# Optimization experiments

Hardware: AMD Instinct MI355X
Metric: run time of the kernel (lower is better)

Reference implementation:

```python
import jax, jax.numpy as jnp
import numpy as np

B, C, H, W, K = 16, 64, 256, 256, 3

def setup_inputs() -> dict:
    key = jax.random.key(0)
    ks = jax.random.split(key, 3)
    x = jax.random.normal(ks[0], (B, C, H, W), dtype=jnp.float32)
    # ReDistribution params
    rd_k = jnp.ones((1, C, 1, 1), jnp.float32)
    rd_b = jnp.zeros((1, C, 1, 1), jnp.float32)
    # Spectral binary activation beta
    beta = jnp.ones((1,), jnp.float32)
    # HardBinaryConv real-valued latent weights (Conv2d default init scale)
    fan_in = C * K * K
    bound = 1.0 / np.sqrt(fan_in)
    conv_w = jax.random.uniform(ks[1], (C, C, K, K), jnp.float32, -bound, bound)
    # RPReLU params
    pr_bias0 = jnp.zeros((1, C, 1, 1), jnp.float32)
    prelu_w = jnp.full((C,), 0.25, jnp.float32)
    pr_bias1 = jnp.zeros((1, C, 1, 1), jnp.float32)
    return {"x": x, "rd_k": rd_k, "rd_b": rd_b, "beta": beta,
            "conv_w": conv_w, "pr_bias0": pr_bias0, "prelu_w": prelu_w,
            "pr_bias1": pr_bias1}

def _ste(hard, soft):
    # straight-through estimator: forward=hard, backward grads flow via soft
    return jax.lax.stop_gradient(hard - soft) + soft

def reference(x, rd_k, rd_b, beta, conv_w, pr_bias0, prelu_w, pr_bias1):
    sg = jax.lax.stop_gradient
    # ReDistribution
    out = x * rd_k + rd_b
    # Spectral binary activation with tanh STE
    out = _ste(jnp.sign(out), jnp.tanh(out * beta))
    # HardBinaryConv: per-output-channel mean |w| scaling, sign binarize, clip STE
    scaling = sg(jnp.mean(jnp.abs(conv_w), axis=(1, 2, 3), keepdims=True))  # [C,1,1,1]
    bw = _ste(scaling * jnp.sign(conv_w), jnp.clip(conv_w, -1.0, 1.0))
    y = jax.lax.conv_general_dilated(
        out, bw, window_strides=(1, 1), padding=((1, 1), (1, 1)),
        dimension_numbers=("NCHW", "OIHW", "NCHW"))
    # RPReLU: bias0 -> per-channel PReLU -> bias1
    y = y + pr_bias0
    y = jnp.where(y >= 0, y, prelu_w[None, :, None, None] * y)
    y = y + pr_bias1
    return y + x
```

## Files before the change

### kernel.cpp

```cpp
#include <hip/hip_runtime.h>
#include <cstdint>
#include <cstddef>

#define Bn 16
#define Cn 64
#define Hn 256
#define Wn 256
#define HWn (Hn * Wn)
#define TH 8
#define ROWS (TH + 2)
#define COLS (Wn + 2)
#define NBLK (Bn * (Hn / TH))
#define THREADS 1024

typedef unsigned long long u64;
typedef u64   u64x2 __attribute__((ext_vector_type(2)));
typedef float f32x2 __attribute__((ext_vector_type(2)));
typedef float f32x4 __attribute__((ext_vector_type(4)));

__global__ __launch_bounds__(64) void pack_weights(const float* __restrict__ w,
                                                   const float* __restrict__ b0g,
                                                   const float* __restrict__ pwg,
                                                   const float* __restrict__ b1g,
                                                   u64* __restrict__ wbits,
                                                   float4* __restrict__ par,
                                                   int* __restrict__ corrx) {
    const int co = blockIdx.x;
    const int ci = threadIdx.x;
    const float* wp = w + ((size_t)co * Cn + ci) * 9;
    float v[9];
    float asum = 0.f;
    #pragma unroll
    for (int t = 0; t < 9; ++t) { v[t] = wp[t]; asum += fabsf(v[t]); }
    u64 m[9];
    #pragma unroll
    for (int t = 0; t < 9; ++t) m[t] = __ballot(v[t] > 0.f);
    #pragma unroll
    for (int off = 32; off; off >>= 1) asum += __shfl_xor(asum, off);
    if (ci == 0) {
        int c[9];
        #pragma unroll
        for (int t = 0; t < 9; ++t) {
            wbits[co * 9 + t] = m[t];
            c[t] = 64 - 2 * (int)__popcll(m[t]);
        }
        int* cx = corrx + co * 8;
        cx[0] = c[0] + c[1] + c[2];
        cx[1] = c[6] + c[7] + c[8];
        cx[2] = c[0] + c[3] + c[6];
        cx[3] = c[2] + c[5] + c[8];
        cx[4] = c[0]; cx[5] = c[2];
        cx[6] = c[6]; cx[7] = c[8];
        par[co] = make_float4(asum * (1.f / (Cn * 9)), b0g[co], pwg[co], b1g[co]);
    }
}

__global__ __launch_bounds__(THREADS, 2) void fused(const float* __restrict__ x,
                                                    const float* __restrict__ rdk,
                                                    const float* __restrict__ rdb,
                                                    const u64* __restrict__ wbits,
                                                    const float4* __restrict__ par,
                                                    const int* __restrict__ corrx,
                                                    float* __restrict__ out) {
    __shared__ __align__(16) u64 s_a[ROWS][COLS];
    __shared__ float2 s_rd[Cn];

    const int tid = threadIdx.x;
    const int bid     = blockIdx.x;
    const int logical = (bid & 7) * (NBLK / 8) + (bid >> 3);
    const int n  = logical >> 5;
    const int h0 = (logical & 31) * TH;

    if (tid < Cn) s_rd[tid] = make_float2(rdk[tid], rdb[tid]);
    if (tid < 2 * ROWS) s_a[tid >> 1][(tid & 1) ? (COLS - 1) : 0] = 0;
    __syncthreads();

    const float* xn = x + (size_t)n * Cn * HWn;
    if (tid < 640) {
        const int r  = tid >> 6;
        const int q  = tid & 63;
        const int gh = h0 - 1 + r;
        const int gw = 4 * q;
        u64 b0 = 0, b1 = 0, b2 = 0, b3 = 0;
        if (gh >= 0 && gh < Hn) {
            const float* xp = xn + (size_t)gh * Wn + gw;
            #pragma unroll 8
            for (int ci = 0; ci < Cn; ++ci) {
                const float2 kb = s_rd[ci];
                const f32x4 v = *reinterpret_cast<const f32x4*>(xp + (size_t)ci * HWn);
                const u64 bit = 1ull << ci;
                if (fmaf(v.x, kb.x, kb.y) > 0.f) b0 |= bit;
                if (fmaf(v.y, kb.x, kb.y) > 0.f) b1 |= bit;
                if (fmaf(v.z, kb.x, kb.y) > 0.f) b2 |= bit;
                if (fmaf(v.w, kb.x, kb.y) > 0.f) b3 |= bit;
            }
        }
        s_a[r][1 + gw] = b0;
        s_a[r][2 + gw] = b1;
        s_a[r][3 + gw] = b2;
        s_a[r][4 + gw] = b3;
    }
    __syncthreads();

    const int r  = tid >> 7;
    const int c0 = (tid & 127) * 2;
    const int h  = h0 + r;
    const int htop = (h == 0), hbot = (h == Hn - 1);
    const int wl = (c0 == 0), wr = (c0 == Wn - 2);
    const int need = htop | hbot | wl | wr;

    const float* xp = x   + (size_t)n * Cn * HWn + (size_t)h * Wn + c0;
    float*       op = out + (size_t)n * Cn * HWn + (size_t)h * Wn + c0;

    const u64* ap = &s_a[r][c0];
    for (int co0 = 0; co0 < Cn; co0 += 4) {
        asm volatile("" : "+v"(ap));
        u64 A[3][4];
        #pragma unroll
        for (int dh = 0; dh < 3; ++dh) {
            const u64x2 t0 = *reinterpret_cast<const u64x2*>(ap + dh * COLS);
            const u64x2 t1 = *reinterpret_cast<const u64x2*>(ap + dh * COLS + 2);
            A[dh][0] = t0.x; A[dh][1] = t0.y; A[dh][2] = t1.x; A[dh][3] = t1.y;
        }
        f32x2 xq[4];
        #pragma unroll
        for (int j = 0; j < 4; ++j)
            xq[j] = *reinterpret_cast<const f32x2*>(xp + (size_t)(co0 + j) * HWn);

        #pragma unroll
        for (int j = 0; j < 4; ++j) {
            const int co = co0 + j;
            const u64* wb = wbits + co * 9;
            int a0 = 0, a1 = 0;
            #pragma unroll
            for (int dh = 0; dh < 3; ++dh) {
                const u64 q0 = wb[dh * 3], q1 = wb[dh * 3 + 1], q2 = wb[dh * 3 + 2];
                a0 += (int)__popcll(A[dh][0] ^ q0) + (int)__popcll(A[dh][1] ^ q1)
                    + (int)__popcll(A[dh][2] ^ q2);
                a1 += (int)__popcll(A[dh][1] ^ q0) + (int)__popcll(A[dh][2] ^ q1)
                    + (int)__popcll(A[dh][3] ^ q2);
            }
            int is0 = 576 - 2 * a0, is1 = 576 - 2 * a1;

            if (need) {
                const int* cx = corrx + co * 8;
                const int sb = (htop ? cx[0] : 0) + (hbot ? cx[1] : 0);
                is0 -= sb; is1 -= sb;
                if (wl) is0 -= cx[2] - (htop ? cx[4] : 0) - (hbot ? cx[6] : 0);
                if (wr) is1 -= cx[3] - (htop ? cx[5] : 0) - (hbot ? cx[7] : 0);
            }

            const float4 p4 = par[co];
            float y0 = fmaf(p4.x, (float)is0, p4.y);
            y0 = (y0 >= 0.f) ? y0 : y0 * p4.z;
            float y1 = fmaf(p4.x, (float)is1, p4.y);
            y1 = (y1 >= 0.f) ? y1 : y1 * p4.z;
            f32x2 o = { y0 + p4.w + xq[j].x, y1 + p4.w + xq[j].y };
            __builtin_nontemporal_store(o, reinterpret_cast<f32x2*>(op + (size_t)co * HWn));
        }
    }
}

extern "C" void kernel_launch(void* const* d_in, const int* in_sizes, int n_in,
                              void* d_out, int out_size, void* d_ws, size_t ws_size,
                              hipStream_t stream) {
    const float* x      = (const float*)d_in[0];
    const float* rd_k   = (const float*)d_in[1];
    const float* rd_b   = (const float*)d_in[2];
    const float* conv_w = (const float*)d_in[4];
    const float* pb0    = (const float*)d_in[5];
    const float* pw     = (const float*)d_in[6];
    const float* pb1    = (const float*)d_in[7];
    float* out = (float*)d_out;

    uint8_t* ws = (uint8_t*)d_ws;
    u64*    wbits = (u64*)ws;
    float4* par   = (float4*)(ws + 4608);
    int*    corrx = (int*)(ws + 4608 + 1024);

    pack_weights<<<Cn, 64, 0, stream>>>(conv_w, pb0, pw, pb1, wbits, par, corrx);
    fused<<<NBLK, THREADS, 0, stream>>>(x, rd_k, rd_b, wbits, par, corrx, out);
}
```

Baseline: 163.9 us.

## Overlap second-half input packing with first-half binary conv compute

The prologue now packs only the first 6 halo rows into the shared bit tile. The remaining 4 rows are packed by every wave, interleaved with the popcount convolution of output rows 0-3, and then a barrier precedes rows 4-7. Work is also remapped so each wave covers 4 rows, a 128-column group and half of the output channels, with wave-uniform indices made scalar via readfirstlane. The aim is to hide the serial packing phase behind compute, at the cost of an extra barrier and scalar per-pixel loads during packing.

```diff
diff --git a/kernel.cpp b/kernel.cpp
--- a/kernel.cpp
+++ b/kernel.cpp
@@ -65,7 +65,10 @@
     __shared__ __align__(16) u64 s_a[ROWS][COLS];
     __shared__ float2 s_rd[Cn];
 
-    const int tid = threadIdx.x;
+    const int tid  = threadIdx.x;
+    const int w_id = tid >> 6;
+    const int lane = tid & 63;
+
     const int bid     = blockIdx.x;
     const int logical = (bid & 7) * (NBLK / 8) + (bid >> 3);
     const int n  = logical >> 5;
@@ -76,7 +79,8 @@
     __syncthreads();
 
     const float* xn = x + (size_t)n * Cn * HWn;
-    if (tid < 640) {
+
+    if (tid < 384) {
         const int r  = tid >> 6;
         const int q  = tid & 63;
         const int gh = h0 - 1 + r;
@@ -102,63 +106,98 @@
     }
     __syncthreads();
 
-    const int r  = tid >> 7;
-    const int c0 = (tid & 127) * 2;
-    const int h  = h0 + r;
-    const int htop = (h == 0), hbot = (h == Hn - 1);
+    const int rsub     = __builtin_amdgcn_readfirstlane(w_id >> 2);
+    const int colgroup = __builtin_amdgcn_readfirstlane((w_id >> 1) & 1);
+    const int half     = __builtin_amdgcn_readfirstlane(w_id & 1);
+    const int c0 = colgroup * 128 + lane * 2;
     const int wl = (c0 == 0), wr = (c0 == Wn - 2);
-    const int need = htop | hbot | wl | wr;
-
-    const float* xp = x   + (size_t)n * Cn * HWn + (size_t)h * Wn + c0;
-    float*       op = out + (size_t)n * Cn * HWn + (size_t)h * Wn + c0;
-
-    const u64* ap = &s_a[r][c0];
-    for (int co0 = 0; co0 < Cn; co0 += 4) {
-        asm volatile("" : "+v"(ap));
-        u64 A[3][4];
-        #pragma unroll
-        for (int dh = 0; dh < 3; ++dh) {
-            const u64x2 t0 = *reinterpret_cast<const u64x2*>(ap + dh * COLS);
-            const u64x2 t1 = *reinterpret_cast<const u64x2*>(ap + dh * COLS + 2);
-            A[dh][0] = t0.x; A[dh][1] = t0.y; A[dh][2] = t1.x; A[dh][3] = t1.y;
-        }
-        f32x2 xq[4];
-        #pragma unroll
-        for (int j = 0; j < 4; ++j)
-            xq[j] = *reinterpret_cast<const f32x2*>(xp + (size_t)(co0 + j) * HWn);
-
-        #pragma unroll
-        for (int j = 0; j < 4; ++j) {
-            const int co = co0 + j;
-            const u64* wb = wbits + co * 9;
-            int a0 = 0, a1 = 0;
+
+    const int prow = 6 + (w_id >> 2);
+    const int pgh  = h0 + 5 + (w_id >> 2);
+    const int ppx  = (w_id & 3) * 64 + lane;
+    const int pgh_c = (pgh < Hn) ? pgh : (Hn - 1);
+    const float* pxp = xn + (size_t)pgh_c * Wn + ppx;
+    u64 pb = 0;
+
+    const int co_lo = half * 32;
+
+    auto conv4 = [&](int rbase, bool do_pack) {
+        const int r = rbase + rsub;
+        const int h = h0 + r;
+        const int htop = (h == 0), hbot = (h == Hn - 1);
+        const int need = htop | hbot | wl | wr;
+
+        const float* xp = xn + (size_t)h * Wn + c0;
+        float*       op = out + (size_t)n * Cn * HWn + (size_t)h * Wn + c0;
+
+        const u64* ap = &s_a[r][c0];
+        for (int i = 0; i < 8; ++i) {
+            if (do_pack) {
+                #pragma unroll
+                for (int k = 0; k < 8; ++k) {
+                    const int ci = 8 * i + k;
+                    const float2 kb = s_rd[ci];
+                    const float v = pxp[(size_t)ci * HWn];
+                    if (fmaf(v, kb.x, kb.y) > 0.f) pb |= 1ull << ci;
+                }
+            }
+
+            asm volatile("" : "+v"(ap));
+            u64 A[3][4];
             #pragma unroll
             for (int dh = 0; dh < 3; ++dh) {
-                const u64 q0 = wb[dh * 3], q1 = wb[dh * 3 + 1], q2 = wb[dh * 3 + 2];
-                a0 += (int)__popcll(A[dh][0] ^ q0) + (int)__popcll(A[dh][1] ^ q1)
-                    + (int)__popcll(A[dh][2] ^ q2);
-                a1 += (int)__popcll(A[dh][1] ^ q0) + (int)__popcll(A[dh][2] ^ q1)
-                    + (int)__popcll(A[dh][3] ^ q2);
-            }
-            int is0 = 576 - 2 * a0, is1 = 576 - 2 * a1;
-
-            if (need) {
-                const int* cx = corrx + co * 8;
-                const int sb = (htop ? cx[0] : 0) + (hbot ? cx[1] : 0);
-                is0 -= sb; is1 -= sb;
-                if (wl) is0 -= cx[2] - (htop ? cx[4] : 0) - (hbot ? cx[6] : 0);
-                if (wr) is1 -= cx[3] - (htop ? cx[5] : 0) - (hbot ? cx[7] : 0);
-            }
-
-            const float4 p4 = par[co];
-            float y0 = fmaf(p4.x, (float)is0, p4.y);
-            y0 = (y0 >= 0.f) ? y0 : y0 * p4.z;
-            float y1 = fmaf(p4.x, (float)is1, p4.y);
-            y1 = (y1 >= 0.f) ? y1 : y1 * p4.z;
-            f32x2 o = { y0 + p4.w + xq[j].x, y1 + p4.w + xq[j].y };
-            __builtin_nontemporal_store(o, reinterpret_cast<f32x2*>(op + (size_t)co * HWn));
+                const u64x2 t0 = *reinterpret_cast<const u64x2*>(ap + dh * COLS);
+                const u64x2 t1 = *reinterpret_cast<const u64x2*>(ap + dh * COLS + 2);
+                A[dh][0] = t0.x; A[dh][1] = t0.y; A[dh][2] = t1.x; A[dh][3] = t1.y;
+            }
+
+            const int co0 = co_lo + 4 * i;
+            f32x2 xq[4];
+            #pragma unroll
+            for (int j = 0; j < 4; ++j)
+                xq[j] = *reinterpret_cast<const f32x2*>(xp + (size_t)(co0 + j) * HWn);
+
+            #pragma unroll
+            for (int j = 0; j < 4; ++j) {
+                const int co = co0 + j;
+                const u64* wb = wbits + co * 9;
+                int a0 = 0, a1 = 0;
+                #pragma unroll
+                for (int dh = 0; dh < 3; ++dh) {
+                    const u64 q0 = wb[dh * 3], q1 = wb[dh * 3 + 1], q2 = wb[dh * 3 + 2];
+                    a0 += (int)__popcll(A[dh][0] ^ q0) + (int)__popcll(A[dh][1] ^ q1)
+                        + (int)__popcll(A[dh][2] ^ q2);
+                    a1 += (int)__popcll(A[dh][1] ^ q0) + (int)__popcll(A[dh][2] ^ q1)
+                        + (int)__popcll(A[dh][3] ^ q2);
+                }
+                int is0 = 576 - 2 * a0, is1 = 576 - 2 * a1;
+
+                if (need) {
+                    const int* cx = corrx + co * 8;
+                    const int sb = (htop ? cx[0] : 0) + (hbot ? cx[1] : 0);
+                    is0 -= sb; is1 -= sb;
+                    if (wl) is0 -= cx[2] - (htop ? cx[4] : 0) - (hbot ? cx[6] : 0);
+                    if (wr) is1 -= cx[3] - (htop ? cx[5] : 0) - (hbot ? cx[7] : 0);
+                }
+
+                const float4 p4 = par[co];
+                float y0 = fmaf(p4.x, (float)is0, p4.y);
+                y0 = (y0 >= 0.f) ? y0 : y0 * p4.z;
+                float y1 = fmaf(p4.x, (float)is1, p4.y);
+                y1 = (y1 >= 0.f) ? y1 : y1 * p4.z;
+                f32x2 o = { y0 + p4.w + xq[j].x, y1 + p4.w + xq[j].y };
+                __builtin_nontemporal_store(o,
+                    reinterpret_cast<f32x2*>(op + (size_t)co * HWn));
+            }
         }
-    }
+    };
+
+    conv4(0, true);
+
+    s_a[prow][1 + ppx] = (pgh < Hn) ? pb : 0;
+    __syncthreads();
+
+    conv4(4, false);
 }
 
 extern "C" void kernel_launch(void* const* d_in, const int* in_sizes, int n_in,
```

New measurement: 163.9 us. About the same (+0.0%).
